# Optimization experiments

Hardware: AMD Instinct MI355X
Metric: run time of the kernel (lower is better)

Reference implementation:

```python
import jax, jax.numpy as jnp
import numpy as np

N_NODES = 2048
IN_FEAT = 128
N_HEADS = 4
N_HIDDEN = 16  # out_features // n_heads = 64 // 4
NEG_SLOPE = 0.2


def setup_inputs() -> dict:
    key = jax.random.key(0)
    k1, k2, k3, k4, k5 = jax.random.split(key, 5)
    h = jax.random.normal(k1, (N_NODES, IN_FEAT), dtype=jnp.float32)
    adj_mat = jax.random.randint(k2, (N_NODES, N_NODES, 1), 0, 2, dtype=jnp.int32)
    scale_w = 1.0 / np.sqrt(IN_FEAT)
    W_l = jax.random.normal(k3, (IN_FEAT, N_HEADS * N_HIDDEN), dtype=jnp.float32) * scale_w
    W_r = jax.random.normal(k4, (IN_FEAT, N_HEADS * N_HIDDEN), dtype=jnp.float32) * scale_w
    attn_w = jax.random.normal(k5, (N_HIDDEN,), dtype=jnp.float32) / np.sqrt(N_HIDDEN)
    return {"h": h, "adj_mat": adj_mat, "W_l": W_l, "W_r": W_r, "attn_w": attn_w}


def reference(h, adj_mat, W_l, W_r, attn_w):
    n = h.shape[0]
    g_l = (h @ W_l).reshape(n, N_HEADS, N_HIDDEN)  # source-side proj
    g_r = (h @ W_r).reshape(n, N_HEADS, N_HIDDEN)  # target-side proj
    # g_sum[i, j, h, f] = g_r[i] + g_l[j]  (matches repeat / repeat_interleave in torch)
    g_sum = g_r[:, None, :, :] + g_l[None, :, :, :]  # [N, N, H, F]
    e = jnp.einsum('ijhf,f->ijh', jax.nn.leaky_relu(g_sum, NEG_SLOPE), attn_w)
    e = jnp.where(adj_mat == 0, -jnp.inf, e)
    a = jnp.nan_to_num(jax.nn.softmax(e, axis=1))  # softmax over neighbors j
    attn_res = jnp.einsum('ijh,jhf->ihf', a, g_r)
    return attn_res.reshape(n, N_HEADS * N_HIDDEN)  # is_concat=True
```

## Files before the change

### kernel.cpp

```cpp
#include <hip/hip_runtime.h>
#include <math.h>
#include <stdint.h>

#define NN 2048
#define IF 128
#define NH 4
#define NF 16
#define OF 64
#define JS 2
#define JT 16
#define NPB 16
#define LOG2E 1.44269504f
#define THR2 11.5417f

typedef float f32x4 __attribute__((ext_vector_type(4)));

__device__ __forceinline__ float rfl(float x) {
    return __int_as_float(__builtin_amdgcn_readfirstlane(__float_as_int(x)));
}
__device__ __forceinline__ void gl2lds16(const void* g, void* l) {
    __builtin_amdgcn_global_load_lds((const __attribute__((address_space(1))) void*)g,
                                     (__attribute__((address_space(3))) void*)l, 16, 0, 0);
}
__device__ __forceinline__ void gl2lds4(const void* g, void* l) {
    __builtin_amdgcn_global_load_lds((const __attribute__((address_space(1))) void*)g,
                                     (__attribute__((address_space(3))) void*)l, 4, 0, 0);
}

__global__ __launch_bounds__(256) void pack_kernel(const int* __restrict__ adj,
                                                   uint32_t* __restrict__ bits) {
    const int w = threadIdx.x >> 6, lane = threadIdx.x & 63;
    const int i = blockIdx.x * 4 + w;
    const int* row = adj + (size_t)i * NN;
    uint64_t*  dst = (uint64_t*)bits + (size_t)i * 32;
    #pragma unroll 4
    for (int k = 0; k < 32; ++k) {
        const int v = row[k * 64 + lane];
        const uint64_t msk = __ballot(v != 0);
        if (lane == 0) dst[k] = msk;
    }
}

__global__ __launch_bounds__(256) void proj_kernel(const float* __restrict__ h,
                                                   const float* __restrict__ Wl,
                                                   const float* __restrict__ Wr,
                                                   const float* __restrict__ attn_w,
                                                   float* __restrict__ glt,
                                                   float* __restrict__ grt,
                                                   float* __restrict__ cj6,
                                                   float* __restrict__ bi6) {
    const int t    = threadIdx.x;
    const int w    = t >> 6, lane = t & 63;
    const int il   = w >> 1, which = w & 1;
    const int i    = blockIdx.x * 2 + il;

    __shared__ float hs[2][IF];
    hs[t >> 7][t & 127] = h[(blockIdx.x * 2 + (t >> 7)) * IF + (t & 127)];
    __syncthreads();

    const float* W = which ? Wr : Wl;
    float acc = 0.f;
    #pragma unroll
    for (int k = 0; k < IF; ++k)
        acc = fmaf(hs[il][k], W[k * OF + lane], acc);

    float* g = which ? grt : glt;
    g[(lane >> 4) * (NN * NF) + i * NF + (lane & 15)] = acc;

    float v = acc * attn_w[lane & 15];
    v += __shfl_xor(v, 1);
    v += __shfl_xor(v, 2);
    v += __shfl_xor(v, 4);
    v += __shfl_xor(v, 8);
    if ((lane & 15) == 0) {
        float* dst = which ? bi6 : cj6;
        dst[(lane >> 4) * NN + i] = 0.6f * LOG2E * v;
    }
}

__global__ __launch_bounds__(256) __attribute__((amdgpu_waves_per_eu(2, 4)))
void gat_kernel(const float* __restrict__ glt,
                const float* __restrict__ grt,
                const float* __restrict__ cj6,
                const float* __restrict__ bi6,
                const uint32_t* __restrict__ bits,
                const float* __restrict__ attn_w,
                float* __restrict__ part) {
    const int t    = threadIdx.x;
    const int wid  = t >> 6, lane = t & 63;
    const int h    = blockIdx.x & 3;
    const int grp  = (blockIdx.x >> 2) & 127;
    const int s    = blockIdx.x >> 9;

    __shared__ __attribute__((aligned(16))) float g_s[2][64 * NF];
    __shared__ __attribute__((aligned(16))) float r_s[2][64 * NF];
    __shared__ uint32_t bits_s[NPB * 32];
    __shared__ float    c_all[JT * 64];
    __shared__ float    red[4][16][NF + 1];

    #pragma unroll
    for (int k = 0; k < 2; ++k) {
        const int f = wid * 128 + k * 64 + lane;
        gl2lds4(bits + ((size_t)(grp * 16 + (f >> 5))) * 64 + s * 32 + (f & 31),
                (char*)bits_s + (wid * 128 + k * 64) * 4);
    }
    {
        const float* cjh = cj6 + h * NN + s * (JT * 64);
        #pragma unroll
        for (int k = 0; k < 4; ++k)
            gl2lds4(cjh + wid * 256 + k * 64 + lane,
                    (char*)c_all + (wid * 256 + k * 64) * 4);
    }

    float aw_s[NF];
    #pragma unroll
    for (int f = 0; f < NF; ++f) aw_s[f] = rfl(attn_w[f]) * (0.4f * LOG2E);
    float gi_s[4][NF], bi_s[4];
    #pragma unroll
    for (int n = 0; n < 4; ++n) {
        const int i_n = grp * 16 + wid * 4 + n;
        #pragma unroll
        for (int f = 0; f < NF; ++f)
            gi_s[n][f] = rfl(grt[h * (NN * NF) + i_n * NF + f]);
        bi_s[n] = rfl(bi6[h * NN + i_n]);
    }

    const float* glh = glt + (size_t)h * NN * NF + (size_t)s * JT * 64 * NF;
    const float* grh = grt + (size_t)h * NN * NF + (size_t)s * JT * 64 * NF;

    const int soff = (wid * 16 + (lane >> 2)) * NF + (((lane & 3) ^ ((lane >> 3) & 3)) << 2);

#define STAGE(tile, nb)                                                   \
    {                                                                     \
        gl2lds16(glh + (size_t)(tile) * 64 * NF + soff, &g_s[nb][wid * 16 * NF]); \
        gl2lds16(grh + (size_t)(tile) * 64 * NF + soff, &r_s[nb][wid * 16 * NF]); \
    }

    float m[4], l[4], acc[4][NF];
    #pragma unroll
    for (int n = 0; n < 4; ++n) {
        m[n] = -INFINITY; l[n] = 0.f;
        #pragma unroll
        for (int f = 0; f < NF; ++f) acc[n][f] = 0.f;
    }

    STAGE(0, 0);
    __syncthreads();

    const int sh = lane & 31;
    #pragma unroll 2
    for (int tt = 0; tt < JT; ++tt) {
        const int buf = tt & 1;
        if (tt + 1 < JT) STAGE(tt + 1, buf ^ 1);

        f32x4 rv[4];
        float ss[4] = {0.f, 0.f, 0.f, 0.f};
        #pragma unroll
        for (int q = 0; q < 4; ++q) {
            const int c = q ^ ((lane >> 1) & 3);
            const f32x4 gv = *(const f32x4*)&g_s[buf][lane * NF + c * 4];
            rv[q] = *(const f32x4*)&r_s[buf][lane * NF + c * 4];
            #pragma unroll
            for (int n = 0; n < 4; ++n) {
                ss[n] = fmaf(fabsf(gv[0] + gi_s[n][q * 4 + 0]), aw_s[q * 4 + 0], ss[n]);
                ss[n] = fmaf(fabsf(gv[1] + gi_s[n][q * 4 + 1]), aw_s[q * 4 + 1], ss[n]);
                ss[n] = fmaf(fabsf(gv[2] + gi_s[n][q * 4 + 2]), aw_s[q * 4 + 2], ss[n]);
                ss[n] = fmaf(fabsf(gv[3] + gi_s[n][q * 4 + 3]), aw_s[q * 4 + 3], ss[n]);
            }
        }
        const float cj = c_all[tt * 64 + lane];

        float e[4], fe[4];
        bool  kk[4];
        bool  anyc = false;
        #pragma unroll
        for (int n = 0; n < 4; ++n) {
            e[n]  = ss[n] + (bi_s[n] + cj);
            const uint32_t wb = bits_s[(wid * 4 + n) * 32 + tt * 2 + (lane >> 5)];
            kk[n] = ((wb >> sh) & 1u) != 0u;
            fe[n] = kk[n] ? e[n] : -INFINITY;
            anyc  = anyc || (fe[n] > m[n] + THR2);
        }
        if (__any(anyc)) {
            #pragma unroll
            for (int n = 0; n < 4; ++n) {
                const bool  c  = fe[n] > m[n] + THR2;
                const float al = c ? __builtin_amdgcn_exp2f(m[n] - fe[n]) : 1.f;
                m[n] = c ? fe[n] : m[n];
                l[n] *= al;
                #pragma unroll
                for (int f = 0; f < NF; ++f) acc[n][f] *= al;
            }
        }
        #pragma unroll
        for (int n = 0; n < 4; ++n) {
            const float p = kk[n] ? __builtin_amdgcn_exp2f(e[n] - m[n]) : 0.f;
            l[n] += p;
            #pragma unroll
            for (int q = 0; q < 4; ++q) {
                acc[n][q * 4 + 0] = fmaf(p, rv[q][0], acc[n][q * 4 + 0]);
                acc[n][q * 4 + 1] = fmaf(p, rv[q][1], acc[n][q * 4 + 1]);
                acc[n][q * 4 + 2] = fmaf(p, rv[q][2], acc[n][q * 4 + 2]);
                acc[n][q * 4 + 3] = fmaf(p, rv[q][3], acc[n][q * 4 + 3]);
            }
        }
        __syncthreads();
    }
#undef STAGE

    #pragma unroll
    for (int n = 0; n < 4; ++n) {
        float M = m[n];
        #pragma unroll
        for (int off = 32; off; off >>= 1) M = fmaxf(M, __shfl_xor(M, off));
        const float sc = (m[n] > -INFINITY) ? __builtin_amdgcn_exp2f(m[n] - M) : 0.f;
        float L = l[n] * sc;
        #pragma unroll
        for (int off = 32; off; off >>= 1) L += __shfl_xor(L, off);

        #pragma unroll
        for (int f = 0; f < NF; ++f) {
            float a = acc[n][f] * sc;
            a += __shfl_xor(a, 32);
            a += __shfl_xor(a, 16);
            if (lane < 16) red[wid][lane][f] = a;
        }
        const int i_n = grp * 16 + wid * 4 + n;
        float* P = part + ((size_t)s * NH * NN + (size_t)h * NN + i_n) * 18;
        if (lane < NF) {
            float a = 0.f;
            #pragma unroll
            for (int r = 0; r < 16; ++r) a += red[wid][r][lane];
            P[lane] = a;
        } else if (lane == 16) P[16] = M;
        else if (lane == 17)   P[17] = L;
    }
}

__global__ __launch_bounds__(256) void reduce_kernel(const float* __restrict__ part,
                                                     float* __restrict__ out) {
    const int c  = blockIdx.x * 256 + threadIdx.x;
    const int f  = c & 15;
    const int ih = c >> 4;
    const float* P0 = part + (size_t)ih * 18;
    const float* P1 = part + (size_t)(NH * NN + ih) * 18;
    const float m0 = P0[16], l0 = P0[17];
    const float m1 = P1[16], l1 = P1[17];
    const float M  = fmaxf(m0, m1);
    float o = 0.f;
    if (M > -INFINITY) {
        const float s0 = (m0 > -INFINITY) ? __builtin_amdgcn_exp2f(m0 - M) : 0.f;
        const float s1 = (m1 > -INFINITY) ? __builtin_amdgcn_exp2f(m1 - M) : 0.f;
        const float L  = l0 * s0 + l1 * s1;
        if (L > 0.f) o = (P0[f] * s0 + P1[f] * s1) / L;
    }
    const int i = ih & (NN - 1);
    const int h = ih >> 11;
    out[(size_t)i * OF + h * NF + f] = o;
}

extern "C" void kernel_launch(void* const* d_in, const int* in_sizes, int n_in,
                              void* d_out, int out_size, void* d_ws, size_t ws_size,
                              hipStream_t stream) {
    const float* h      = (const float*)d_in[0];
    const int*   adj    = (const int*)d_in[1];
    const float* W_l    = (const float*)d_in[2];
    const float* W_r    = (const float*)d_in[3];
    const float* attn_w = (const float*)d_in[4];
    float*       out    = (float*)d_out;

    float*    glt  = (float*)d_ws;
    float*    grt  = glt + (size_t)NN * OF;
    float*    cj6  = grt + (size_t)NN * OF;
    float*    bi6  = cj6 + (size_t)NH * NN;
    uint32_t* bits = (uint32_t*)(bi6 + (size_t)NH * NN);
    float*    prt  = (float*)(bits + (size_t)NN * 64);

    pack_kernel<<<NN / 4, 256, 0, stream>>>(adj, bits);
    proj_kernel<<<NN / 2, 256, 0, stream>>>(h, W_l, W_r, attn_w, glt, grt, cj6, bi6);
    gat_kernel<<<JS * 128 * NH, 256, 0, stream>>>(glt, grt, cj6, bi6, bits, attn_w, prt);
    reduce_kernel<<<NH * NN * NF / 256, 256, 0, stream>>>(prt, out);
}
```

Measured before the change: 71.80 us.

## Process eight target rows per wave to reuse staged tiles, packed FMA

Each wave now handles eight target nodes instead of four, which doubles the rows per block and halves the grid size. Each LDS tile of g_l and g_r is therefore reused across twice as many rows. The accumulators become float2 vectors so the weighted sum can use packed FMA, and the online-softmax rescale check now runs per row. The extra rows raise register pressure (four rows kept in uniform registers, four in vector registers), occupancy is pinned at 2 waves per EU, and the smaller grid of 512 blocks may underfill the GPU's compute units.

```diff
diff --git a/kernel.cpp b/kernel.cpp
--- a/kernel.cpp
+++ b/kernel.cpp
@@ -9,10 +9,12 @@
 #define OF 64
 #define JS 2
 #define JT 16
-#define NPB 16
+#define NPW 8
+#define NPB 32
 #define LOG2E 1.44269504f
 #define THR2 11.5417f
 
+typedef float f32x2 __attribute__((ext_vector_type(2)));
 typedef float f32x4 __attribute__((ext_vector_type(4)));
 
 __device__ __forceinline__ float rfl(float x) {
@@ -78,7 +80,7 @@
     }
 }
 
-__global__ __launch_bounds__(256) __attribute__((amdgpu_waves_per_eu(2, 4)))
+__global__ __launch_bounds__(256) __attribute__((amdgpu_waves_per_eu(2, 2)))
 void gat_kernel(const float* __restrict__ glt,
                 const float* __restrict__ grt,
                 const float* __restrict__ cj6,
@@ -89,8 +91,8 @@
     const int t    = threadIdx.x;
     const int wid  = t >> 6, lane = t & 63;
     const int h    = blockIdx.x & 3;
-    const int grp  = (blockIdx.x >> 2) & 127;
-    const int s    = blockIdx.x >> 9;
+    const int grp  = (blockIdx.x >> 2) & 63;
+    const int s    = blockIdx.x >> 8;
 
     __shared__ __attribute__((aligned(16))) float g_s[2][64 * NF];
     __shared__ __attribute__((aligned(16))) float r_s[2][64 * NF];
@@ -99,30 +101,49 @@
     __shared__ float    red[4][16][NF + 1];
 
     #pragma unroll
-    for (int k = 0; k < 2; ++k) {
-        const int f = wid * 128 + k * 64 + lane;
-        gl2lds4(bits + ((size_t)(grp * 16 + (f >> 5))) * 64 + s * 32 + (f & 31),
-                (char*)bits_s + (wid * 128 + k * 64) * 4);
+    for (int k = 0; k < 4; ++k) {
+        const int idx = k * 256 + wid * 64 + lane;
+        gl2lds4(bits + ((size_t)(grp * 32 + (idx >> 5))) * 64 + s * 32 + (idx & 31),
+                (char*)bits_s + (k * 256 + wid * 64) * 4);
     }
     {
         const float* cjh = cj6 + h * NN + s * (JT * 64);
         #pragma unroll
         for (int k = 0; k < 4; ++k)
-            gl2lds4(cjh + wid * 256 + k * 64 + lane,
-                    (char*)c_all + (wid * 256 + k * 64) * 4);
+            gl2lds4(cjh + k * 256 + wid * 64 + lane,
+                    (char*)c_all + (k * 256 + wid * 64) * 4);
     }
 
     float aw_s[NF];
     #pragma unroll
     for (int f = 0; f < NF; ++f) aw_s[f] = rfl(attn_w[f]) * (0.4f * LOG2E);
-    float gi_s[4][NF], bi_s[4];
+
+    const float* gbase = grt + (size_t)h * NN * NF;
+    const int ib = grp * NPB + wid * NPW;
+    float gi_s[4][NF], gi_v[4][NF], bi_s[8];
     #pragma unroll
     for (int n = 0; n < 4; ++n) {
-        const int i_n = grp * 16 + wid * 4 + n;
-        #pragma unroll
-        for (int f = 0; f < NF; ++f)
-            gi_s[n][f] = rfl(grt[h * (NN * NF) + i_n * NF + f]);
-        bi_s[n] = rfl(bi6[h * NN + i_n]);
+        #pragma unroll
+        for (int q = 0; q < 4; ++q) {
+            const f32x4 v = *(const f32x4*)(gbase + (size_t)(ib + n) * NF + q * 4);
+            gi_s[n][q * 4 + 0] = rfl(v[0]);
+            gi_s[n][q * 4 + 1] = rfl(v[1]);
+            gi_s[n][q * 4 + 2] = rfl(v[2]);
+            gi_s[n][q * 4 + 3] = rfl(v[3]);
+        }
+        bi_s[n] = rfl(bi6[h * NN + ib + n]);
+    }
+    #pragma unroll
+    for (int n = 0; n < 4; ++n) {
+        #pragma unroll
+        for (int q = 0; q < 4; ++q) {
+            const f32x4 v = *(const f32x4*)(gbase + (size_t)(ib + 4 + n) * NF + q * 4);
+            gi_v[n][q * 4 + 0] = v[0];
+            gi_v[n][q * 4 + 1] = v[1];
+            gi_v[n][q * 4 + 2] = v[2];
+            gi_v[n][q * 4 + 3] = v[3];
+        }
+        bi_s[4 + n] = rfl(bi6[h * NN + ib + 4 + n]);
     }
 
     const float* glh = glt + (size_t)h * NN * NF + (size_t)s * JT * 64 * NF;
@@ -136,30 +157,28 @@
         gl2lds16(grh + (size_t)(tile) * 64 * NF + soff, &r_s[nb][wid * 16 * NF]); \
     }
 
-    float m[4], l[4], acc[4][NF];
-    #pragma unroll
-    for (int n = 0; n < 4; ++n) {
+    float m[NPW], l[NPW];
+    f32x2 acc[NPW][8];
+    #pragma unroll
+    for (int n = 0; n < NPW; ++n) {
         m[n] = -INFINITY; l[n] = 0.f;
         #pragma unroll
-        for (int f = 0; f < NF; ++f) acc[n][f] = 0.f;
+        for (int k = 0; k < 8; ++k) acc[n][k] = (f32x2){0.f, 0.f};
     }
 
     STAGE(0, 0);
     __syncthreads();
 
     const int sh = lane & 31;
-    #pragma unroll 2
     for (int tt = 0; tt < JT; ++tt) {
         const int buf = tt & 1;
         if (tt + 1 < JT) STAGE(tt + 1, buf ^ 1);
 
-        f32x4 rv[4];
-        float ss[4] = {0.f, 0.f, 0.f, 0.f};
+        float ss[NPW] = {0.f, 0.f, 0.f, 0.f, 0.f, 0.f, 0.f, 0.f};
         #pragma unroll
         for (int q = 0; q < 4; ++q) {
             const int c = q ^ ((lane >> 1) & 3);
             const f32x4 gv = *(const f32x4*)&g_s[buf][lane * NF + c * 4];
-            rv[q] = *(const f32x4*)&r_s[buf][lane * NF + c * 4];
             #pragma unroll
             for (int n = 0; n < 4; ++n) {
                 ss[n] = fmaf(fabsf(gv[0] + gi_s[n][q * 4 + 0]), aw_s[q * 4 + 0], ss[n]);
@@ -167,41 +186,48 @@
                 ss[n] = fmaf(fabsf(gv[2] + gi_s[n][q * 4 + 2]), aw_s[q * 4 + 2], ss[n]);
                 ss[n] = fmaf(fabsf(gv[3] + gi_s[n][q * 4 + 3]), aw_s[q * 4 + 3], ss[n]);
             }
-        }
-        const float cj = c_all[tt * 64 + lane];
-
-        float e[4], fe[4];
-        bool  kk[4];
-        bool  anyc = false;
-        #pragma unroll
-        for (int n = 0; n < 4; ++n) {
-            e[n]  = ss[n] + (bi_s[n] + cj);
-            const uint32_t wb = bits_s[(wid * 4 + n) * 32 + tt * 2 + (lane >> 5)];
-            kk[n] = ((wb >> sh) & 1u) != 0u;
-            fe[n] = kk[n] ? e[n] : -INFINITY;
-            anyc  = anyc || (fe[n] > m[n] + THR2);
-        }
-        if (__any(anyc)) {
             #pragma unroll
             for (int n = 0; n < 4; ++n) {
-                const bool  c  = fe[n] > m[n] + THR2;
-                const float al = c ? __builtin_amdgcn_exp2f(m[n] - fe[n]) : 1.f;
-                m[n] = c ? fe[n] : m[n];
+                ss[4 + n] = fmaf(fabsf(gv[0] + gi_v[n][q * 4 + 0]), aw_s[q * 4 + 0], ss[4 + n]);
+                ss[4 + n] = fmaf(fabsf(gv[1] + gi_v[n][q * 4 + 1]), aw_s[q * 4 + 1], ss[4 + n]);
+                ss[4 + n] = fmaf(fabsf(gv[2] + gi_v[n][q * 4 + 2]), aw_s[q * 4 + 2], ss[4 + n]);
+                ss[4 + n] = fmaf(fabsf(gv[3] + gi_v[n][q * 4 + 3]), aw_s[q * 4 + 3], ss[4 + n]);
+            }
+        }
+        const float cj = c_all[tt * 64 + lane];
+
+        float p[NPW];
+        #pragma unroll
+        for (int n = 0; n < NPW; ++n) {
+            const float e = ss[n] + (bi_s[n] + cj);
+            const uint32_t wb = bits_s[(wid * NPW + n) * 32 + tt * 2 + (lane >> 5)];
+            const bool  kk = ((wb >> sh) & 1u) != 0u;
+            const float fe = kk ? e : -INFINITY;
+            if (__any(fe > m[n] + THR2)) {
+                const bool  c  = fe > m[n] + THR2;
+                const float al = c ? __builtin_amdgcn_exp2f(m[n] - fe) : 1.f;
+                m[n] = c ? fe : m[n];
                 l[n] *= al;
+                const f32x2 a2 = {al, al};
                 #pragma unroll
-                for (int f = 0; f < NF; ++f) acc[n][f] *= al;
+                for (int k = 0; k < 8; ++k) acc[n][k] *= a2;
             }
-        }
-        #pragma unroll
-        for (int n = 0; n < 4; ++n) {
-            const float p = kk[n] ? __builtin_amdgcn_exp2f(e[n] - m[n]) : 0.f;
-            l[n] += p;
+            const float pp = kk ? __builtin_amdgcn_exp2f(e - m[n]) : 0.f;
+            l[n] += pp;
+            p[n] = pp;
+        }
+
+        #pragma unroll
+        for (int q = 0; q < 4; ++q) {
+            const int c = q ^ ((lane >> 1) & 3);
+            const f32x4 rv = *(const f32x4*)&r_s[buf][lane * NF + c * 4];
+            const f32x2 lo = {rv[0], rv[1]};
+            const f32x2 hi = {rv[2], rv[3]};
             #pragma unroll
-            for (int q = 0; q < 4; ++q) {
-                acc[n][q * 4 + 0] = fmaf(p, rv[q][0], acc[n][q * 4 + 0]);
-                acc[n][q * 4 + 1] = fmaf(p, rv[q][1], acc[n][q * 4 + 1]);
-                acc[n][q * 4 + 2] = fmaf(p, rv[q][2], acc[n][q * 4 + 2]);
-                acc[n][q * 4 + 3] = fmaf(p, rv[q][3], acc[n][q * 4 + 3]);
+            for (int n = 0; n < NPW; ++n) {
+                const f32x2 pp2 = {p[n], p[n]};
+                acc[n][q * 2 + 0] = __builtin_elementwise_fma(pp2, lo, acc[n][q * 2 + 0]);
+                acc[n][q * 2 + 1] = __builtin_elementwise_fma(pp2, hi, acc[n][q * 2 + 1]);
             }
         }
         __syncthreads();
@@ -209,7 +235,7 @@
 #undef STAGE
 
     #pragma unroll
-    for (int n = 0; n < 4; ++n) {
+    for (int n = 0; n < NPW; ++n) {
         float M = m[n];
         #pragma unroll
         for (int off = 32; off; off >>= 1) M = fmaxf(M, __shfl_xor(M, off));
@@ -220,12 +246,12 @@
 
         #pragma unroll
         for (int f = 0; f < NF; ++f) {
-            float a = acc[n][f] * sc;
+            float a = acc[n][f >> 1][f & 1] * sc;
             a += __shfl_xor(a, 32);
             a += __shfl_xor(a, 16);
             if (lane < 16) red[wid][lane][f] = a;
         }
-        const int i_n = grp * 16 + wid * 4 + n;
+        const int i_n = ib + n;
         float* P = part + ((size_t)s * NH * NN + (size_t)h * NN + i_n) * 18;
         if (lane < NF) {
             float a = 0.f;
@@ -278,6 +304,6 @@
 
     pack_kernel<<<NN / 4, 256, 0, stream>>>(adj, bits);
     proj_kernel<<<NN / 2, 256, 0, stream>>>(h, W_l, W_r, attn_w, glt, grt, cj6, bi6);
-    gat_kernel<<<JS * 128 * NH, 256, 0, stream>>>(glt, grt, cj6, bi6, bits, attn_w, prt);
+    gat_kernel<<<JS * 64 * NH, 256, 0, stream>>>(glt, grt, cj6, bi6, bits, attn_w, prt);
     reduce_kernel<<<NH * NN * NF / 256, 256, 0, stream>>>(prt, out);
 }
```

Result: slower. 85.93 us (+19.7%).

## Replace online softmax max-tracking with precomputed per-row upper bound

Applied to the files above, without the earlier changes.

Per-row softmax shifts now come from an upper bound on the logits, built from |g|·|attn_w| terms computed in the projection kernel plus a new tiny kernel that takes the per-head max over j. The GAT loop drops the running max, the conditional rescaling branch and the max merge in the reduce step, and uses packed f32x2 FMAs for the accumulation. The bias term that is constant per row is dropped because it cancels in the softmax. The cost is an extra kernel launch, and underflow can occur if the bound is much looser than the true row max.

```diff
diff --git a/kernel.cpp b/kernel.cpp
--- a/kernel.cpp
+++ b/kernel.cpp
@@ -11,8 +11,8 @@
 #define JT 16
 #define NPB 16
 #define LOG2E 1.44269504f
-#define THR2 11.5417f
-
+
+typedef float f32x2 __attribute__((ext_vector_type(2)));
 typedef float f32x4 __attribute__((ext_vector_type(4)));
 
 __device__ __forceinline__ float rfl(float x) {
@@ -48,7 +48,8 @@
                                                    float* __restrict__ glt,
                                                    float* __restrict__ grt,
                                                    float* __restrict__ cj6,
-                                                   float* __restrict__ bi6) {
+                                                   float* __restrict__ cjB,
+                                                   float* __restrict__ ai2) {
     const int t    = threadIdx.x;
     const int w    = t >> 6, lane = t & 63;
     const int il   = w >> 1, which = w & 1;
@@ -67,22 +68,45 @@
     float* g = which ? grt : glt;
     g[(lane >> 4) * (NN * NF) + i * NF + (lane & 15)] = acc;
 
-    float v = acc * attn_w[lane & 15];
-    v += __shfl_xor(v, 1);
-    v += __shfl_xor(v, 2);
-    v += __shfl_xor(v, 4);
-    v += __shfl_xor(v, 8);
+    const float awv = attn_w[lane & 15];
+    float v  = acc * awv;
+    float vb = fabsf(acc) * fabsf(awv);
+    #pragma unroll
+    for (int off = 1; off <= 8; off <<= 1) {
+        v  += __shfl_xor(v,  off);
+        vb += __shfl_xor(vb, off);
+    }
     if ((lane & 15) == 0) {
-        float* dst = which ? bi6 : cj6;
-        dst[(lane >> 4) * NN + i] = 0.6f * LOG2E * v;
-    }
+        const int hh = lane >> 4;
+        if (which) {
+            ai2[hh * NN + i] = 0.4f * LOG2E * vb;
+        } else {
+            const float c2 = 0.6f * LOG2E * v;
+            cj6[hh * NN + i] = c2;
+            cjB[hh * NN + i] = fmaf(0.4f * LOG2E, vb, c2);
+        }
+    }
+}
+
+__global__ __launch_bounds__(256) void mh_kernel(const float* __restrict__ cjB,
+                                                 float* __restrict__ mh) {
+    const int hh = blockIdx.x, t = threadIdx.x;
+    float mx = -INFINITY;
+    for (int j = t; j < NN; j += 256) mx = fmaxf(mx, cjB[hh * NN + j]);
+    #pragma unroll
+    for (int off = 32; off; off >>= 1) mx = fmaxf(mx, __shfl_xor(mx, off));
+    __shared__ float wmx[4];
+    if ((t & 63) == 0) wmx[t >> 6] = mx;
+    __syncthreads();
+    if (t == 0) mh[hh] = fmaxf(fmaxf(wmx[0], wmx[1]), fmaxf(wmx[2], wmx[3]));
 }
 
 __global__ __launch_bounds__(256) __attribute__((amdgpu_waves_per_eu(2, 4)))
 void gat_kernel(const float* __restrict__ glt,
                 const float* __restrict__ grt,
                 const float* __restrict__ cj6,
-                const float* __restrict__ bi6,
+                const float* __restrict__ ai2,
+                const float* __restrict__ mh,
                 const uint32_t* __restrict__ bits,
                 const float* __restrict__ attn_w,
                 float* __restrict__ part) {
@@ -108,21 +132,22 @@
         const float* cjh = cj6 + h * NN + s * (JT * 64);
         #pragma unroll
         for (int k = 0; k < 4; ++k)
-            gl2lds4(cjh + wid * 256 + k * 64 + lane,
-                    (char*)c_all + (wid * 256 + k * 64) * 4);
+            gl2lds4(cjh + k * 256 + wid * 64 + lane,
+                    (char*)c_all + (k * 256 + wid * 64) * 4);
     }
 
     float aw_s[NF];
     #pragma unroll
     for (int f = 0; f < NF; ++f) aw_s[f] = rfl(attn_w[f]) * (0.4f * LOG2E);
-    float gi_s[4][NF], bi_s[4];
+    const float mh_s = rfl(mh[h]);
+    float gi_s[4][NF], cni[4];
     #pragma unroll
     for (int n = 0; n < 4; ++n) {
         const int i_n = grp * 16 + wid * 4 + n;
         #pragma unroll
         for (int f = 0; f < NF; ++f)
             gi_s[n][f] = rfl(grt[h * (NN * NF) + i_n * NF + f]);
-        bi_s[n] = rfl(bi6[h * NN + i_n]);
+        cni[n] = -(rfl(ai2[h * NN + i_n]) + mh_s);
     }
 
     const float* glh = glt + (size_t)h * NN * NF + (size_t)s * JT * 64 * NF;
@@ -136,12 +161,13 @@
         gl2lds16(grh + (size_t)(tile) * 64 * NF + soff, &r_s[nb][wid * 16 * NF]); \
     }
 
-    float m[4], l[4], acc[4][NF];
+    float l[4];
+    f32x2 acc[4][8];
     #pragma unroll
     for (int n = 0; n < 4; ++n) {
-        m[n] = -INFINITY; l[n] = 0.f;
-        #pragma unroll
-        for (int f = 0; f < NF; ++f) acc[n][f] = 0.f;
+        l[n] = 0.f;
+        #pragma unroll
+        for (int k = 0; k < 8; ++k) acc[n][k] = (f32x2){0.f, 0.f};
     }
 
     STAGE(0, 0);
@@ -170,57 +196,42 @@
         }
         const float cj = c_all[tt * 64 + lane];
 
-        float e[4], fe[4];
-        bool  kk[4];
-        bool  anyc = false;
+        float p[4];
         #pragma unroll
         for (int n = 0; n < 4; ++n) {
-            e[n]  = ss[n] + (bi_s[n] + cj);
             const uint32_t wb = bits_s[(wid * 4 + n) * 32 + tt * 2 + (lane >> 5)];
-            kk[n] = ((wb >> sh) & 1u) != 0u;
-            fe[n] = kk[n] ? e[n] : -INFINITY;
-            anyc  = anyc || (fe[n] > m[n] + THR2);
-        }
-        if (__any(anyc)) {
+            const bool  kk = ((wb >> sh) & 1u) != 0u;
+            float e = (ss[n] + cj) + cni[n];
+            e = kk ? e : -INFINITY;
+            const float pp = __builtin_amdgcn_exp2f(e);
+            l[n] += pp;
+            p[n] = pp;
+        }
+
+        #pragma unroll
+        for (int q = 0; q < 4; ++q) {
+            const f32x2 lo = {rv[q][0], rv[q][1]};
+            const f32x2 hi = {rv[q][2], rv[q][3]};
             #pragma unroll
             for (int n = 0; n < 4; ++n) {
-                const bool  c  = fe[n] > m[n] + THR2;
-                const float al = c ? __builtin_amdgcn_exp2f(m[n] - fe[n]) : 1.f;
-                m[n] = c ? fe[n] : m[n];
-                l[n] *= al;
-                #pragma unroll
-                for (int f = 0; f < NF; ++f) acc[n][f] *= al;
+                const f32x2 pp2 = {p[n], p[n]};
+                acc[n][q * 2 + 0] = __builtin_elementwise_fma(pp2, lo, acc[n][q * 2 + 0]);
+                acc[n][q * 2 + 1] = __builtin_elementwise_fma(pp2, hi, acc[n][q * 2 + 1]);
             }
         }
-        #pragma unroll
-        for (int n = 0; n < 4; ++n) {
-            const float p = kk[n] ? __builtin_amdgcn_exp2f(e[n] - m[n]) : 0.f;
-            l[n] += p;
-            #pragma unroll
-            for (int q = 0; q < 4; ++q) {
-                acc[n][q * 4 + 0] = fmaf(p, rv[q][0], acc[n][q * 4 + 0]);
-                acc[n][q * 4 + 1] = fmaf(p, rv[q][1], acc[n][q * 4 + 1]);
-                acc[n][q * 4 + 2] = fmaf(p, rv[q][2], acc[n][q * 4 + 2]);
-                acc[n][q * 4 + 3] = fmaf(p, rv[q][3], acc[n][q * 4 + 3]);
-            }
-        }
         __syncthreads();
     }
 #undef STAGE
 
     #pragma unroll
     for (int n = 0; n < 4; ++n) {
-        float M = m[n];
-        #pragma unroll
-        for (int off = 32; off; off >>= 1) M = fmaxf(M, __shfl_xor(M, off));
-        const float sc = (m[n] > -INFINITY) ? __builtin_amdgcn_exp2f(m[n] - M) : 0.f;
-        float L = l[n] * sc;
+        float L = l[n];
         #pragma unroll
         for (int off = 32; off; off >>= 1) L += __shfl_xor(L, off);
 
         #pragma unroll
         for (int f = 0; f < NF; ++f) {
-            float a = acc[n][f] * sc;
+            float a = acc[n][f >> 1][f & 1];
             a += __shfl_xor(a, 32);
             a += __shfl_xor(a, 16);
             if (lane < 16) red[wid][lane][f] = a;
@@ -232,8 +243,7 @@
             #pragma unroll
             for (int r = 0; r < 16; ++r) a += red[wid][r][lane];
             P[lane] = a;
-        } else if (lane == 16) P[16] = M;
-        else if (lane == 17)   P[17] = L;
+        } else if (lane == 16) P[16] = L;
     }
 }
 
@@ -244,16 +254,8 @@
     const int ih = c >> 4;
     const float* P0 = part + (size_t)ih * 18;
     const float* P1 = part + (size_t)(NH * NN + ih) * 18;
-    const float m0 = P0[16], l0 = P0[17];
-    const float m1 = P1[16], l1 = P1[17];
-    const float M  = fmaxf(m0, m1);
-    float o = 0.f;
-    if (M > -INFINITY) {
-        const float s0 = (m0 > -INFINITY) ? __builtin_amdgcn_exp2f(m0 - M) : 0.f;
-        const float s1 = (m1 > -INFINITY) ? __builtin_amdgcn_exp2f(m1 - M) : 0.f;
-        const float L  = l0 * s0 + l1 * s1;
-        if (L > 0.f) o = (P0[f] * s0 + P1[f] * s1) / L;
-    }
+    const float L = P0[16] + P1[16];
+    const float o = (L > 0.f) ? (P0[f] + P1[f]) / L : 0.f;
     const int i = ih & (NN - 1);
     const int h = ih >> 11;
     out[(size_t)i * OF + h * NF + f] = o;
@@ -272,12 +274,15 @@
     float*    glt  = (float*)d_ws;
     float*    grt  = glt + (size_t)NN * OF;
     float*    cj6  = grt + (size_t)NN * OF;
-    float*    bi6  = cj6 + (size_t)NH * NN;
-    uint32_t* bits = (uint32_t*)(bi6 + (size_t)NH * NN);
+    float*    cjB  = cj6 + (size_t)NH * NN;
+    float*    ai2  = cjB + (size_t)NH * NN;
+    float*    mh   = ai2 + (size_t)NH * NN;
+    uint32_t* bits = (uint32_t*)(mh + 64);
     float*    prt  = (float*)(bits + (size_t)NN * 64);
 
     pack_kernel<<<NN / 4, 256, 0, stream>>>(adj, bits);
-    proj_kernel<<<NN / 2, 256, 0, stream>>>(h, W_l, W_r, attn_w, glt, grt, cj6, bi6);
-    gat_kernel<<<JS * 128 * NH, 256, 0, stream>>>(glt, grt, cj6, bi6, bits, attn_w, prt);
+    proj_kernel<<<NN / 2, 256, 0, stream>>>(h, W_l, W_r, attn_w, glt, grt, cj6, cjB, ai2);
+    mh_kernel<<<NH, 256, 0, stream>>>(cjB, mh);
+    gat_kernel<<<JS * 128 * NH, 256, 0, stream>>>(glt, grt, cj6, ai2, mh, bits, attn_w, prt);
     reduce_kernel<<<NH * NN * NF / 256, 256, 0, stream>>>(prt, out);
 }
```

Measured after the change: 61.50 us. 1.17x faster.
